# Optimization experiments

Measured on AMD Instinct MI355X. Metric: run time of the kernel, lower is better.

The kernel has to match this reference:

```python
import jax, jax.numpy as jnp
import numpy as np

A_BITS = 8   # activation fake-quant bits
W_BITS = 4   # weight fake-quant bits

H, I = 4096, 11008          # hidden / intermediate (LLaMA-7B)
UP_L, UP_R = 64, 64         # get_decompose_dim(4096)
DN_L, DN_R = 86, 128        # get_decompose_dim(11008)


def _round_ste(x):
    # straight-through rounding (fake quant)
    return x + jax.lax.stop_gradient(jnp.round(x) - x)


def fake_quant(x, bits, axis):
    """Symmetric fake quantization with dynamic max scaling along `axis`."""
    qmax = 2.0 ** (bits - 1) - 1.0
    s = jnp.max(jnp.abs(x), axis=axis, keepdims=True) / qmax
    s = jnp.maximum(s, 1e-8)
    q = jnp.clip(_round_ste(x / s), -qmax - 1.0, qmax)
    return q * s


def kron_trans(x, L, R, diag):
    """FlatQuant Kronecker-decomposed transform: x_ts = (x * diag) @ kron(L, R).
    Implemented as reshape to (l, r), L^T X R, reshape back."""
    shape = x.shape
    l, r = L.shape[0], R.shape[0]
    xr = (x * diag).reshape(*shape[:-1], l, r)
    y = jnp.einsum('...ij,ip,jq->...pq', xr, L, R)  # L^T X R
    return y.reshape(shape)


def inv_trans_weight(W, L, R, diag):
    """Transform weight rows by T^{-T} (T = diag * kron(L,R)) so that
    (x T) @ W_t^T == x @ W^T. W: [out, in]."""
    o, n = W.shape
    l, r = L.shape[0], R.shape[0]
    Wr = (W / diag).reshape(o, l, r)
    Li = jnp.linalg.inv(L)
    Ri = jnp.linalg.inv(R)
    Wt = jnp.einsum('pi,oij,qj->opq', Li, Wr, Ri)  # L^{-1} W' R^{-T}
    return Wt.reshape(o, n)


def setup_inputs() -> dict:
    key = jax.random.key(0)
    ks = jax.random.split(key, 10)
    B, S = 2, 2048

    def ortho(k, n):
        return jnp.linalg.qr(jax.random.normal(k, (n, n), jnp.float32))[0]

    x = jax.random.normal(ks[0], (B, S, H), jnp.float32)
    w_up = jax.random.normal(ks[1], (I, H), jnp.float32) * 0.02
    w_gate = jax.random.normal(ks[2], (I, H), jnp.float32) * 0.02
    w_down = jax.random.normal(ks[3], (H, I), jnp.float32) * 0.02
    up_L = ortho(ks[4], UP_L)
    up_R = ortho(ks[5], UP_R)
    up_diag = jax.random.uniform(ks[6], (H,), jnp.float32, 0.5, 1.5)
    dn_L = ortho(ks[7], DN_L)
    dn_R = ortho(ks[8], DN_R)
    dn_diag = jax.random.uniform(ks[9], (I,), jnp.float32, 0.5, 1.5)
    return {"x": x, "w_up": w_up, "w_gate": w_gate, "w_down": w_down,
            "up_L": up_L, "up_R": up_R, "up_diag": up_diag,
            "dn_L": dn_L, "dn_R": dn_R, "dn_diag": dn_diag}


def reference(x, w_up, w_gate, w_down, up_L, up_R, up_diag, dn_L, dn_R, dn_diag):
    # up/gate branch: transform -> quantize activation -> quantized linears
    x_ts = kron_trans(x, up_L, up_R, up_diag)                 # [B,S,H]
    xq = fake_quant(x_ts, A_BITS, -1)                         # per-token A8
    wu = fake_quant(inv_trans_weight(w_up, up_L, up_R, up_diag), W_BITS, 1)
    wg = fake_quant(inv_trans_weight(w_gate, up_L, up_R, up_diag), W_BITS, 1)
    up = jnp.einsum('bsh,ih->bsi', xq, wu)                    # [B,S,I]
    gate = jnp.einsum('bsh,ih->bsi', xq, wg)
    h = jax.nn.silu(gate) * up                                # SwiGLU
    # down branch
    h_ts = kron_trans(h, dn_L, dn_R, dn_diag)                 # [B,S,I]
    hq = fake_quant(h_ts, A_BITS, -1)
    wd = fake_quant(inv_trans_weight(w_down, dn_L, dn_R, dn_diag), W_BITS, 1)
    return jnp.einsum('bsi,hi->bsh', hq, wd)                  # [B,S,H]
```

## Files before the change

### kernel.cpp

```cpp
#include <hip/hip_runtime.h>
#include <hip/hip_bf16.h>
#include <math.h>

typedef __bf16 bf16x8 __attribute__((ext_vector_type(8)));
typedef float f32x4 __attribute__((ext_vector_type(4)));

#define TOK 4096
#define HDIM 4096
#define IDIM 11008

__global__ __launch_bounds__(256) void t64_kernel(
    const float* __restrict__ src, const float* __restrict__ Lm,
    const float* __restrict__ Rm, const float* __restrict__ diag,
    __hip_bfloat16* __restrict__ outq, float* __restrict__ scales,
    int mulDiag, float qmax, float qlo, float qhi)
{
    __shared__ float X[64 * 68];
    __shared__ float M1[64 * 68];
    __shared__ float LR[64 * 68];
    const int tid = threadIdx.x;
    const int row = blockIdx.x;
    const float* srow = src + (size_t)row * 4096;

    for (int idx = tid; idx < 4096; idx += 256) {
        float d = diag[idx];
        float v = srow[idx];
        v = mulDiag ? v * d : v / d;
        X[(idx >> 6) * 68 + (idx & 63)] = v;
        LR[(idx >> 6) * 68 + (idx & 63)] = Lm[idx];
    }
    __syncthreads();

    const int p0 = (tid >> 4) << 2;
    const int j0 = (tid & 15) << 2;

    float acc[4][4] = {};
    for (int i = 0; i < 64; ++i) {
        float a[4];
#pragma unroll
        for (int ii = 0; ii < 4; ++ii) a[ii] = LR[i * 68 + p0 + ii];
        float4 b = *(const float4*)&X[i * 68 + j0];
        float bv[4] = {b.x, b.y, b.z, b.w};
#pragma unroll
        for (int ii = 0; ii < 4; ++ii)
#pragma unroll
            for (int jj = 0; jj < 4; ++jj) acc[ii][jj] += a[ii] * bv[jj];
    }
#pragma unroll
    for (int ii = 0; ii < 4; ++ii)
        *(float4*)&M1[(p0 + ii) * 68 + j0] =
            make_float4(acc[ii][0], acc[ii][1], acc[ii][2], acc[ii][3]);
    __syncthreads();

    for (int idx = tid; idx < 4096; idx += 256)
        LR[(idx >> 6) * 68 + (idx & 63)] = Rm[idx];
    __syncthreads();

    float acc2[4][4] = {};
    for (int j = 0; j < 64; ++j) {
        float a[4];
#pragma unroll
        for (int ii = 0; ii < 4; ++ii) a[ii] = M1[(p0 + ii) * 68 + j];
        float4 b = *(const float4*)&LR[j * 68 + j0];
        float bv[4] = {b.x, b.y, b.z, b.w};
#pragma unroll
        for (int ii = 0; ii < 4; ++ii)
#pragma unroll
            for (int jj = 0; jj < 4; ++jj) acc2[ii][jj] += a[ii] * bv[jj];
    }

    float lm = 0.f;
#pragma unroll
    for (int ii = 0; ii < 4; ++ii)
#pragma unroll
        for (int jj = 0; jj < 4; ++jj) lm = fmaxf(lm, fabsf(acc2[ii][jj]));
    X[tid] = lm;
    __syncthreads();
    for (int s = 128; s > 0; s >>= 1) {
        if (tid < s) X[tid] = fmaxf(X[tid], X[tid + s]);
        __syncthreads();
    }
    const float sc = fmaxf(X[0] / qmax, 1e-8f);

#pragma unroll
    for (int ii = 0; ii < 4; ++ii)
#pragma unroll
        for (int jj = 0; jj < 4; ++jj) {
            float q = rintf(acc2[ii][jj] / sc);
            q = fminf(fmaxf(q, qlo), qhi);
            outq[(size_t)row * 4096 + (p0 + ii) * 64 + (j0 + jj)] =
                __float2bfloat16(q);
        }
    if (tid == 0) scales[row] = sc;
}

__global__ __launch_bounds__(512) void tdn_kernel(
    const void* __restrict__ src, int srcIsBf16,
    const float* __restrict__ Lm, const float* __restrict__ Rm,
    const float* __restrict__ diag,
    __hip_bfloat16* __restrict__ outq, float* __restrict__ scales,
    int mulDiag, float qmax, float qlo, float qhi)
{
    extern __shared__ float dsm[];
    float* X  = dsm;
    float* M1 = dsm + 11352;
    float* LR = dsm + 22704;
    __shared__ float red[512];

    const int tid = threadIdx.x;
    const int row = blockIdx.x;

    for (int idx = tid; idx < IDIM; idx += 512) {
        float v = srcIsBf16
            ? __bfloat162float(((const __hip_bfloat16*)src)[(size_t)row * IDIM + idx])
            : ((const float*)src)[(size_t)row * IDIM + idx];
        float d = diag[idx];
        v = mulDiag ? v * d : v / d;
        X[(idx >> 7) * 132 + (idx & 127)] = v;
    }
    for (int idx = tid; idx < 86 * 86; idx += 512) {
        int r = idx / 86, c = idx - r * 86;
        LR[r * 88 + c] = Lm[idx];
    }
    __syncthreads();

    for (int tt = tid; tt < 1376; tt += 512) {
        const int pp = (tt >> 5) * 2;
        const int jj0 = (tt & 31) * 4;
        float acc[2][4] = {};
        for (int i = 0; i < 86; ++i) {
            float a0 = LR[i * 88 + pp];
            float a1 = LR[i * 88 + pp + 1];
            float4 b = *(const float4*)&X[i * 132 + jj0];
            acc[0][0] += a0 * b.x; acc[0][1] += a0 * b.y;
            acc[0][2] += a0 * b.z; acc[0][3] += a0 * b.w;
            acc[1][0] += a1 * b.x; acc[1][1] += a1 * b.y;
            acc[1][2] += a1 * b.z; acc[1][3] += a1 * b.w;
        }
        *(float4*)&M1[pp * 132 + jj0] =
            make_float4(acc[0][0], acc[0][1], acc[0][2], acc[0][3]);
        *(float4*)&M1[(pp + 1) * 132 + jj0] =
            make_float4(acc[1][0], acc[1][1], acc[1][2], acc[1][3]);
    }
    __syncthreads();

    for (int idx = tid; idx < 128 * 128; idx += 512) {
        int r = idx >> 7, c = idx & 127;
        LR[r * 132 + c] = Rm[idx];
    }
    __syncthreads();

    float lm = 0.f;
    for (int tt = tid; tt < 1376; tt += 512) {
        const int pp = (tt >> 5) * 2;
        const int q0 = (tt & 31) * 4;
        float acc[2][4] = {};
        for (int j = 0; j < 128; ++j) {
            float a0 = M1[pp * 132 + j];
            float a1 = M1[(pp + 1) * 132 + j];
            float4 b = *(const float4*)&LR[j * 132 + q0];
            acc[0][0] += a0 * b.x; acc[0][1] += a0 * b.y;
            acc[0][2] += a0 * b.z; acc[0][3] += a0 * b.w;
            acc[1][0] += a1 * b.x; acc[1][1] += a1 * b.y;
            acc[1][2] += a1 * b.z; acc[1][3] += a1 * b.w;
        }
        *(float4*)&X[pp * 132 + q0] =
            make_float4(acc[0][0], acc[0][1], acc[0][2], acc[0][3]);
        *(float4*)&X[(pp + 1) * 132 + q0] =
            make_float4(acc[1][0], acc[1][1], acc[1][2], acc[1][3]);
#pragma unroll
        for (int ii = 0; ii < 2; ++ii)
#pragma unroll
            for (int qq = 0; qq < 4; ++qq) lm = fmaxf(lm, fabsf(acc[ii][qq]));
    }
    red[tid] = lm;
    __syncthreads();
    for (int s = 256; s > 0; s >>= 1) {
        if (tid < s) red[tid] = fmaxf(red[tid], red[tid + s]);
        __syncthreads();
    }
    const float sc = fmaxf(red[0] / qmax, 1e-8f);

    for (int idx = tid; idx < IDIM; idx += 512) {
        float v = X[(idx >> 7) * 132 + (idx & 127)];
        float q = rintf(v / sc);
        q = fminf(fmaxf(q, qlo), qhi);
        outq[(size_t)row * IDIM + idx] = __float2bfloat16(q);
    }
    if (tid == 0) scales[row] = sc;
}

__device__ __forceinline__ void gload16(const __hip_bfloat16* gsrc,
                                        __hip_bfloat16* ldst)
{
    __builtin_amdgcn_global_load_lds(
        (const __attribute__((address_space(1))) unsigned int*)gsrc,
        (__attribute__((address_space(3))) unsigned int*)ldst, 16, 0, 0);
}

template <bool DUAL>
__global__ __launch_bounds__(256, 2) void gemm_kernel(
    const __hip_bfloat16* __restrict__ A,
    const __hip_bfloat16* __restrict__ B0,
    const __hip_bfloat16* __restrict__ B1,
    const float* __restrict__ sA,
    const float* __restrict__ sB0,
    const float* __restrict__ sB1,
    int K,
    __hip_bfloat16* __restrict__ outH,
    float* __restrict__ outF,
    int outLd)
{
    constexpr int NT = DUAL ? 3 : 2;
    constexpr int TSZ = 128 * 64;
    __shared__ __align__(16) __hip_bfloat16 smem[NT * TSZ];

    const int tid = threadIdx.x;
    const int lane = tid & 63;
    const int lane15 = lane & 15;
    const int quad = lane >> 4;
    const int wave = tid >> 6;
    const int wr = wave >> 1;
    const int wc = wave & 1;
    const int n0 = blockIdx.x * 128;
    const int m0 = blockIdx.y * 128;

    const int srow = lane >> 3;
    const int scol = (lane & 7) * 8;

    f32x4 acc0[4][4] = {};
    f32x4 acc1[4][4] = {};

    const __hip_bfloat16* gA  = A + (size_t)m0 * K;
    const __hip_bfloat16* gB0 = B0 + (size_t)n0 * K;
    const __hip_bfloat16* gB1 = DUAL ? (B1 + (size_t)n0 * K) : nullptr;

    for (int kk = 0; kk < K; kk += 64) {
#pragma unroll
        for (int c = 0; c < 4; ++c) {
            const int r0 = wave * 32 + c * 8;
            gload16(gA + (size_t)(r0 + srow) * K + kk + scol,
                    smem + r0 * 64);
            gload16(gB0 + (size_t)(r0 + srow) * K + kk + scol,
                    smem + TSZ + r0 * 64);
            if constexpr (DUAL)
                gload16(gB1 + (size_t)(r0 + srow) * K + kk + scol,
                        smem + 2 * TSZ + r0 * 64);
        }
        __syncthreads();

#pragma unroll
        for (int ks = 0; ks < 2; ++ks) {
            const int kb = ks * 32 + quad * 8;
            bf16x8 af[4];
#pragma unroll
            for (int m = 0; m < 4; ++m)
                af[m] = *(const bf16x8*)(smem +
                         (wr * 64 + m * 16 + lane15) * 64 + kb);
#pragma unroll
            for (int c = 0; c < 4; ++c) {
                bf16x8 b0 = *(const bf16x8*)(smem + TSZ +
                             (wc * 64 + c * 16 + lane15) * 64 + kb);
#pragma unroll
                for (int m = 0; m < 4; ++m)
                    acc0[m][c] = __builtin_amdgcn_mfma_f32_16x16x32_bf16(
                        af[m], b0, acc0[m][c], 0, 0, 0);
                if constexpr (DUAL) {
                    bf16x8 b1 = *(const bf16x8*)(smem + 2 * TSZ +
                                 (wc * 64 + c * 16 + lane15) * 64 + kb);
#pragma unroll
                    for (int m = 0; m < 4; ++m)
                        acc1[m][c] = __builtin_amdgcn_mfma_f32_16x16x32_bf16(
                            af[m], b1, acc1[m][c], 0, 0, 0);
                }
            }
        }
        __syncthreads();
    }

#pragma unroll
    for (int m = 0; m < 4; ++m) {
        const int r0 = m0 + wr * 64 + m * 16 + quad * 4;
        float sa[4];
#pragma unroll
        for (int r = 0; r < 4; ++r) sa[r] = sA[r0 + r];
#pragma unroll
        for (int c = 0; c < 4; ++c) {
            const int col = n0 + wc * 64 + c * 16 + lane15;
            if constexpr (DUAL) {
                const float s0 = sB0[col], s1 = sB1[col];
#pragma unroll
                for (int r = 0; r < 4; ++r) {
                    float up = acc0[m][c][r] * (sa[r] * s0);
                    float gt = acc1[m][c][r] * (sa[r] * s1);
                    float hv = up * (gt / (1.f + __expf(-gt)));
                    outH[(size_t)(r0 + r) * outLd + col] = __float2bfloat16(hv);
                }
            } else {
                const float s0 = sB0[col];
#pragma unroll
                for (int r = 0; r < 4; ++r)
                    outF[(size_t)(r0 + r) * outLd + col] =
                        acc0[m][c][r] * (sa[r] * s0);
            }
        }
    }
}

extern "C" void kernel_launch(void* const* d_in, const int* in_sizes, int n_in,
                              void* d_out, int out_size, void* d_ws, size_t ws_size,
                              hipStream_t stream)
{
    const float* x       = (const float*)d_in[0];
    const float* w_up    = (const float*)d_in[1];
    const float* w_gate  = (const float*)d_in[2];
    const float* w_down  = (const float*)d_in[3];
    const float* up_L    = (const float*)d_in[4];
    const float* up_R    = (const float*)d_in[5];
    const float* up_diag = (const float*)d_in[6];
    const float* dn_L    = (const float*)d_in[7];
    const float* dn_R    = (const float*)d_in[8];
    const float* dn_diag = (const float*)d_in[9];
    float* out = (float*)d_out;

    char* w = (char*)d_ws;
    size_t off = 0;
    auto take = [&](size_t b) { char* p = w + off; off += (b + 255) & ~(size_t)255; return p; };
    __hip_bfloat16* wuq = (__hip_bfloat16*)take((size_t)IDIM * HDIM * 2);
    __hip_bfloat16* wgq = (__hip_bfloat16*)take((size_t)IDIM * HDIM * 2);
    __hip_bfloat16* wdq = (__hip_bfloat16*)take((size_t)HDIM * IDIM * 2);
    __hip_bfloat16* xq  = (__hip_bfloat16*)take((size_t)TOK * HDIM * 2);
    __hip_bfloat16* hq  = (__hip_bfloat16*)take((size_t)TOK * IDIM * 2);
    float* sx = (float*)take(TOK * 4);
    float* su = (float*)take(IDIM * 4);
    float* sg = (float*)take(IDIM * 4);
    float* sh = (float*)take(TOK * 4);
    float* sd = (float*)take(HDIM * 4);
    (void)in_sizes; (void)n_in; (void)out_size; (void)ws_size;

    const size_t tdn_lds = (size_t)(11352 + 11352 + 16896) * sizeof(float);
    hipFuncSetAttribute(reinterpret_cast<const void*>(&tdn_kernel),
                        hipFuncAttributeMaxDynamicSharedMemorySize, (int)tdn_lds);

    t64_kernel<<<TOK,  256, 0, stream>>>(x,      up_L, up_R, up_diag, xq,  sx, 1, 127.f, -128.f, 127.f);
    t64_kernel<<<IDIM, 256, 0, stream>>>(w_up,   up_L, up_R, up_diag, wuq, su, 0, 7.f,   -8.f,   7.f);
    t64_kernel<<<IDIM, 256, 0, stream>>>(w_gate, up_L, up_R, up_diag, wgq, sg, 0, 7.f,   -8.f,   7.f);
    tdn_kernel<<<HDIM, 512, tdn_lds, stream>>>(w_down, 0, dn_L, dn_R, dn_diag, wdq, sd, 0, 7.f, -8.f, 7.f);

    gemm_kernel<true><<<dim3(IDIM / 128, TOK / 128), 256, 0, stream>>>(
        xq, wuq, wgq, sx, su, sg, HDIM, hq, nullptr, IDIM);

    tdn_kernel<<<TOK, 512, tdn_lds, stream>>>(hq, 1, dn_L, dn_R, dn_diag, hq, sh, 1, 127.f, -128.f, 127.f);

    gemm_kernel<false><<<dim3(HDIM / 128, TOK / 128), 256, 0, stream>>>(
        hq, wdq, nullptr, sh, sd, nullptr, IDIM, nullptr, out, HDIM);
}
```

Before: 3.586 ms.

## Vectorize and retile Kronecker transform kernels with transposed intermediate layout

Rewrites the per-row Kronecker transform kernels to use float4 global loads and packed bf16 stores. The first-stage result is stored transposed so the second matmul reads float4 operands instead of scalar strided ones. The 11008-wide kernel moves to 256 threads, each computing a 4x8 register tile, which raises arithmetic per LDS load and changes the LDS layout. Register pressure and occupancy trade-offs may shift, and the GEMMs, which likely dominate total time, are unchanged.

```diff
diff --git a/kernel.cpp b/kernel.cpp
--- a/kernel.cpp
+++ b/kernel.cpp
@@ -8,6 +8,14 @@
 #define TOK 4096
 #define HDIM 4096
 #define IDIM 11008
+
+__device__ __forceinline__ unsigned int bf16bits(float f)
+{
+    __hip_bfloat16 h = __float2bfloat16(f);
+    union { __hip_bfloat16 h; unsigned short u; } cv;
+    cv.h = h;
+    return (unsigned int)cv.u;
+}
 
 __global__ __launch_bounds__(256) void t64_kernel(
     const float* __restrict__ src, const float* __restrict__ Lm,
@@ -22,12 +30,16 @@
     const int row = blockIdx.x;
     const float* srow = src + (size_t)row * 4096;
 
-    for (int idx = tid; idx < 4096; idx += 256) {
-        float d = diag[idx];
-        float v = srow[idx];
-        v = mulDiag ? v * d : v / d;
-        X[(idx >> 6) * 68 + (idx & 63)] = v;
-        LR[(idx >> 6) * 68 + (idx & 63)] = Lm[idx];
+    for (int i4 = tid; i4 < 1024; i4 += 256) {
+        const int idx = i4 * 4;
+        float4 d = *(const float4*)(diag + idx);
+        float4 v = *(const float4*)(srow + idx);
+        float4 l = *(const float4*)(Lm + idx);
+        if (mulDiag) { v.x *= d.x; v.y *= d.y; v.z *= d.z; v.w *= d.w; }
+        else         { v.x /= d.x; v.y /= d.y; v.z /= d.z; v.w /= d.w; }
+        const int r = idx >> 6, c = idx & 63;
+        *(float4*)&X[r * 68 + c] = v;
+        *(float4*)&LR[r * 68 + c] = l;
     }
     __syncthreads();
 
@@ -35,38 +47,36 @@
     const int j0 = (tid & 15) << 2;
 
     float acc[4][4] = {};
+#pragma unroll 2
     for (int i = 0; i < 64; ++i) {
-        float a[4];
-#pragma unroll
-        for (int ii = 0; ii < 4; ++ii) a[ii] = LR[i * 68 + p0 + ii];
+        float4 a = *(const float4*)&LR[i * 68 + p0];
         float4 b = *(const float4*)&X[i * 68 + j0];
-        float bv[4] = {b.x, b.y, b.z, b.w};
-#pragma unroll
-        for (int ii = 0; ii < 4; ++ii)
-#pragma unroll
-            for (int jj = 0; jj < 4; ++jj) acc[ii][jj] += a[ii] * bv[jj];
-    }
-#pragma unroll
-    for (int ii = 0; ii < 4; ++ii)
-        *(float4*)&M1[(p0 + ii) * 68 + j0] =
-            make_float4(acc[ii][0], acc[ii][1], acc[ii][2], acc[ii][3]);
-    __syncthreads();
-
-    for (int idx = tid; idx < 4096; idx += 256)
-        LR[(idx >> 6) * 68 + (idx & 63)] = Rm[idx];
+        acc[0][0] += a.x * b.x; acc[0][1] += a.x * b.y; acc[0][2] += a.x * b.z; acc[0][3] += a.x * b.w;
+        acc[1][0] += a.y * b.x; acc[1][1] += a.y * b.y; acc[1][2] += a.y * b.z; acc[1][3] += a.y * b.w;
+        acc[2][0] += a.z * b.x; acc[2][1] += a.z * b.y; acc[2][2] += a.z * b.z; acc[2][3] += a.z * b.w;
+        acc[3][0] += a.w * b.x; acc[3][1] += a.w * b.y; acc[3][2] += a.w * b.z; acc[3][3] += a.w * b.w;
+    }
+#pragma unroll
+    for (int jj = 0; jj < 4; ++jj)
+        *(float4*)&M1[(j0 + jj) * 68 + p0] =
+            make_float4(acc[0][jj], acc[1][jj], acc[2][jj], acc[3][jj]);
+    __syncthreads();
+
+    for (int i4 = tid; i4 < 1024; i4 += 256) {
+        const int idx = i4 * 4;
+        *(float4*)&LR[(idx >> 6) * 68 + (idx & 63)] = *(const float4*)(Rm + idx);
+    }
     __syncthreads();
 
     float acc2[4][4] = {};
+#pragma unroll 2
     for (int j = 0; j < 64; ++j) {
-        float a[4];
-#pragma unroll
-        for (int ii = 0; ii < 4; ++ii) a[ii] = M1[(p0 + ii) * 68 + j];
+        float4 a = *(const float4*)&M1[j * 68 + p0];
         float4 b = *(const float4*)&LR[j * 68 + j0];
-        float bv[4] = {b.x, b.y, b.z, b.w};
-#pragma unroll
-        for (int ii = 0; ii < 4; ++ii)
-#pragma unroll
-            for (int jj = 0; jj < 4; ++jj) acc2[ii][jj] += a[ii] * bv[jj];
+        acc2[0][0] += a.x * b.x; acc2[0][1] += a.x * b.y; acc2[0][2] += a.x * b.z; acc2[0][3] += a.x * b.w;
+        acc2[1][0] += a.y * b.x; acc2[1][1] += a.y * b.y; acc2[1][2] += a.y * b.z; acc2[1][3] += a.y * b.w;
+        acc2[2][0] += a.z * b.x; acc2[2][1] += a.z * b.y; acc2[2][2] += a.z * b.z; acc2[2][3] += a.z * b.w;
+        acc2[3][0] += a.w * b.x; acc2[3][1] += a.w * b.y; acc2[3][2] += a.w * b.z; acc2[3][3] += a.w * b.w;
     }
 
     float lm = 0.f;
@@ -83,18 +93,23 @@
     const float sc = fmaxf(X[0] / qmax, 1e-8f);
 
 #pragma unroll
-    for (int ii = 0; ii < 4; ++ii)
-#pragma unroll
-        for (int jj = 0; jj < 4; ++jj) {
-            float q = rintf(acc2[ii][jj] / sc);
-            q = fminf(fmaxf(q, qlo), qhi);
-            outq[(size_t)row * 4096 + (p0 + ii) * 64 + (j0 + jj)] =
-                __float2bfloat16(q);
-        }
+    for (int ii = 0; ii < 4; ++ii) {
+        unsigned int lo, hi;
+        {
+            float q0 = fminf(fmaxf(rintf(acc2[ii][0] / sc), qlo), qhi);
+            float q1 = fminf(fmaxf(rintf(acc2[ii][1] / sc), qlo), qhi);
+            float q2 = fminf(fmaxf(rintf(acc2[ii][2] / sc), qlo), qhi);
+            float q3 = fminf(fmaxf(rintf(acc2[ii][3] / sc), qlo), qhi);
+            lo = bf16bits(q0) | (bf16bits(q1) << 16);
+            hi = bf16bits(q2) | (bf16bits(q3) << 16);
+        }
+        *(uint2*)(outq + (size_t)row * 4096 + (p0 + ii) * 64 + j0) =
+            make_uint2(lo, hi);
+    }
     if (tid == 0) scales[row] = sc;
 }
 
-__global__ __launch_bounds__(512) void tdn_kernel(
+__global__ __launch_bounds__(256) void tdn_kernel(
     const void* __restrict__ src, int srcIsBf16,
     const float* __restrict__ Lm, const float* __restrict__ Rm,
     const float* __restrict__ diag,
@@ -103,89 +118,115 @@
 {
     extern __shared__ float dsm[];
     float* X  = dsm;
-    float* M1 = dsm + 11352;
-    float* LR = dsm + 22704;
-    __shared__ float red[512];
+    float* M1 = dsm + 11616;
+    float* LR = dsm + 22880;
+    __shared__ float red[256];
 
     const int tid = threadIdx.x;
     const int row = blockIdx.x;
 
-    for (int idx = tid; idx < IDIM; idx += 512) {
-        float v = srcIsBf16
-            ? __bfloat162float(((const __hip_bfloat16*)src)[(size_t)row * IDIM + idx])
-            : ((const float*)src)[(size_t)row * IDIM + idx];
-        float d = diag[idx];
-        v = mulDiag ? v * d : v / d;
-        X[(idx >> 7) * 132 + (idx & 127)] = v;
-    }
-    for (int idx = tid; idx < 86 * 86; idx += 512) {
-        int r = idx / 86, c = idx - r * 86;
-        LR[r * 88 + c] = Lm[idx];
-    }
-    __syncthreads();
-
-    for (int tt = tid; tt < 1376; tt += 512) {
-        const int pp = (tt >> 5) * 2;
-        const int jj0 = (tt & 31) * 4;
-        float acc[2][4] = {};
+    for (int i4 = tid; i4 < IDIM / 4; i4 += 256) {
+        const int idx = i4 * 4;
+        float4 v;
+        if (srcIsBf16) {
+            uint2 raw = *(const uint2*)((const unsigned short*)src +
+                                        (size_t)row * IDIM + idx);
+            v.x = __uint_as_float(raw.x << 16);
+            v.y = __uint_as_float(raw.x & 0xffff0000u);
+            v.z = __uint_as_float(raw.y << 16);
+            v.w = __uint_as_float(raw.y & 0xffff0000u);
+        } else {
+            v = *(const float4*)((const float*)src + (size_t)row * IDIM + idx);
+        }
+        float4 d = *(const float4*)(diag + idx);
+        if (mulDiag) { v.x *= d.x; v.y *= d.y; v.z *= d.z; v.w *= d.w; }
+        else         { v.x /= d.x; v.y /= d.y; v.z /= d.z; v.w /= d.w; }
+        *(float4*)&X[(idx >> 7) * 132 + (idx & 127)] = v;
+    }
+    for (int idx = tid; idx < 86 * 88; idx += 256) {
+        const int r = idx / 88, c = idx - r * 88;
+        LR[idx] = (c < 86) ? Lm[r * 86 + c] : 0.f;
+    }
+    __syncthreads();
+
+    for (int tt = tid; tt < 352; tt += 256) {
+        const int pp = (tt >> 4) << 2;
+        const int jb = (tt & 15) << 3;
+        float acc[4][8] = {};
+#pragma unroll 2
         for (int i = 0; i < 86; ++i) {
-            float a0 = LR[i * 88 + pp];
-            float a1 = LR[i * 88 + pp + 1];
-            float4 b = *(const float4*)&X[i * 132 + jj0];
-            acc[0][0] += a0 * b.x; acc[0][1] += a0 * b.y;
-            acc[0][2] += a0 * b.z; acc[0][3] += a0 * b.w;
-            acc[1][0] += a1 * b.x; acc[1][1] += a1 * b.y;
-            acc[1][2] += a1 * b.z; acc[1][3] += a1 * b.w;
-        }
-        *(float4*)&M1[pp * 132 + jj0] =
-            make_float4(acc[0][0], acc[0][1], acc[0][2], acc[0][3]);
-        *(float4*)&M1[(pp + 1) * 132 + jj0] =
-            make_float4(acc[1][0], acc[1][1], acc[1][2], acc[1][3]);
-    }
-    __syncthreads();
-
-    for (int idx = tid; idx < 128 * 128; idx += 512) {
-        int r = idx >> 7, c = idx & 127;
-        LR[r * 132 + c] = Rm[idx];
+            float4 a  = *(const float4*)&LR[i * 88 + pp];
+            float4 b0 = *(const float4*)&X[i * 132 + jb];
+            float4 b1 = *(const float4*)&X[i * 132 + jb + 4];
+            acc[0][0] += a.x * b0.x; acc[0][1] += a.x * b0.y; acc[0][2] += a.x * b0.z; acc[0][3] += a.x * b0.w;
+            acc[0][4] += a.x * b1.x; acc[0][5] += a.x * b1.y; acc[0][6] += a.x * b1.z; acc[0][7] += a.x * b1.w;
+            acc[1][0] += a.y * b0.x; acc[1][1] += a.y * b0.y; acc[1][2] += a.y * b0.z; acc[1][3] += a.y * b0.w;
+            acc[1][4] += a.y * b1.x; acc[1][5] += a.y * b1.y; acc[1][6] += a.y * b1.z; acc[1][7] += a.y * b1.w;
+            acc[2][0] += a.z * b0.x; acc[2][1] += a.z * b0.y; acc[2][2] += a.z * b0.z; acc[2][3] += a.z * b0.w;
+            acc[2][4] += a.z * b1.x; acc[2][5] += a.z * b1.y; acc[2][6] += a.z * b1.z; acc[2][7] += a.z * b1.w;
+            acc[3][0] += a.w * b0.x; acc[3][1] += a.w * b0.y; acc[3][2] += a.w * b0.z; acc[3][3] += a.w * b0.w;
+            acc[3][4] += a.w * b1.x; acc[3][5] += a.w * b1.y; acc[3][6] += a.w * b1.z; acc[3][7] += a.w * b1.w;
+        }
+#pragma unroll
+        for (int jj = 0; jj < 8; ++jj)
+            *(float4*)&M1[(jb + jj) * 88 + pp] =
+                make_float4(acc[0][jj], acc[1][jj], acc[2][jj], acc[3][jj]);
+    }
+    __syncthreads();
+
+    for (int i4 = tid; i4 < 4096; i4 += 256) {
+        const int idx = i4 * 4;
+        *(float4*)&LR[(idx >> 7) * 132 + (idx & 127)] = *(const float4*)(Rm + idx);
     }
     __syncthreads();
 
     float lm = 0.f;
-    for (int tt = tid; tt < 1376; tt += 512) {
-        const int pp = (tt >> 5) * 2;
-        const int q0 = (tt & 31) * 4;
-        float acc[2][4] = {};
+    for (int tt = tid; tt < 352; tt += 256) {
+        const int pp = (tt >> 4) << 2;
+        const int qb = (tt & 15) << 3;
+        float acc[4][8] = {};
+#pragma unroll 2
         for (int j = 0; j < 128; ++j) {
-            float a0 = M1[pp * 132 + j];
-            float a1 = M1[(pp + 1) * 132 + j];
-            float4 b = *(const float4*)&LR[j * 132 + q0];
-            acc[0][0] += a0 * b.x; acc[0][1] += a0 * b.y;
-            acc[0][2] += a0 * b.z; acc[0][3] += a0 * b.w;
-            acc[1][0] += a1 * b.x; acc[1][1] += a1 * b.y;
-            acc[1][2] += a1 * b.z; acc[1][3] += a1 * b.w;
-        }
-        *(float4*)&X[pp * 132 + q0] =
-            make_float4(acc[0][0], acc[0][1], acc[0][2], acc[0][3]);
-        *(float4*)&X[(pp + 1) * 132 + q0] =
-            make_float4(acc[1][0], acc[1][1], acc[1][2], acc[1][3]);
-#pragma unroll
-        for (int ii = 0; ii < 2; ++ii)
-#pragma unroll
-            for (int qq = 0; qq < 4; ++qq) lm = fmaxf(lm, fabsf(acc[ii][qq]));
+            float4 a  = *(const float4*)&M1[j * 88 + pp];
+            float4 b0 = *(const float4*)&LR[j * 132 + qb];
+            float4 b1 = *(const float4*)&LR[j * 132 + qb + 4];
+            acc[0][0] += a.x * b0.x; acc[0][1] += a.x * b0.y; acc[0][2] += a.x * b0.z; acc[0][3] += a.x * b0.w;
+            acc[0][4] += a.x * b1.x; acc[0][5] += a.x * b1.y; acc[0][6] += a.x * b1.z; acc[0][7] += a.x * b1.w;
+            acc[1][0] += a.y * b0.x; acc[1][1] += a.y * b0.y; acc[1][2] += a.y * b0.z; acc[1][3] += a.y * b0.w;
+            acc[1][4] += a.y * b1.x; acc[1][5] += a.y * b1.y; acc[1][6] += a.y * b1.z; acc[1][7] += a.y * b1.w;
+            acc[2][0] += a.z * b0.x; acc[2][1] += a.z * b0.y; acc[2][2] += a.z * b0.z; acc[2][3] += a.z * b0.w;
+            acc[2][4] += a.z * b1.x; acc[2][5] += a.z * b1.y; acc[2][6] += a.z * b1.z; acc[2][7] += a.z * b1.w;
+            acc[3][0] += a.w * b0.x; acc[3][1] += a.w * b0.y; acc[3][2] += a.w * b0.z; acc[3][3] += a.w * b0.w;
+            acc[3][4] += a.w * b1.x; acc[3][5] += a.w * b1.y; acc[3][6] += a.w * b1.z; acc[3][7] += a.w * b1.w;
+        }
+#pragma unroll
+        for (int ii = 0; ii < 4; ++ii) {
+            *(float4*)&X[(pp + ii) * 132 + qb] =
+                make_float4(acc[ii][0], acc[ii][1], acc[ii][2], acc[ii][3]);
+            *(float4*)&X[(pp + ii) * 132 + qb + 4] =
+                make_float4(acc[ii][4], acc[ii][5], acc[ii][6], acc[ii][7]);
+#pragma unroll
+            for (int qq = 0; qq < 8; ++qq) lm = fmaxf(lm, fabsf(acc[ii][qq]));
+        }
     }
     red[tid] = lm;
     __syncthreads();
-    for (int s = 256; s > 0; s >>= 1) {
+    for (int s = 128; s > 0; s >>= 1) {
         if (tid < s) red[tid] = fmaxf(red[tid], red[tid + s]);
         __syncthreads();
     }
     const float sc = fmaxf(red[0] / qmax, 1e-8f);
 
-    for (int idx = tid; idx < IDIM; idx += 512) {
-        float v = X[(idx >> 7) * 132 + (idx & 127)];
-        float q = rintf(v / sc);
-        q = fminf(fmaxf(q, qlo), qhi);
-        outq[(size_t)row * IDIM + idx] = __float2bfloat16(q);
+    for (int i4 = tid; i4 < IDIM / 4; i4 += 256) {
+        const int idx = i4 * 4;
+        float4 v = *(const float4*)&X[(idx >> 7) * 132 + (idx & 127)];
+        float q0 = fminf(fmaxf(rintf(v.x / sc), qlo), qhi);
+        float q1 = fminf(fmaxf(rintf(v.y / sc), qlo), qhi);
+        float q2 = fminf(fmaxf(rintf(v.z / sc), qlo), qhi);
+        float q3 = fminf(fmaxf(rintf(v.w / sc), qlo), qhi);
+        unsigned int lo = bf16bits(q0) | (bf16bits(q1) << 16);
+        unsigned int hi = bf16bits(q2) | (bf16bits(q3) << 16);
+        *(uint2*)(outq + (size_t)row * IDIM + idx) = make_uint2(lo, hi);
     }
     if (tid == 0) scales[row] = sc;
 }
@@ -338,19 +379,19 @@
     float* sd = (float*)take(HDIM * 4);
     (void)in_sizes; (void)n_in; (void)out_size; (void)ws_size;
 
-    const size_t tdn_lds = (size_t)(11352 + 11352 + 16896) * sizeof(float);
+    const size_t tdn_lds = (size_t)(11616 + 11264 + 16896) * sizeof(float);
     hipFuncSetAttribute(reinterpret_cast<const void*>(&tdn_kernel),
                         hipFuncAttributeMaxDynamicSharedMemorySize, (int)tdn_lds);
 
     t64_kernel<<<TOK,  256, 0, stream>>>(x,      up_L, up_R, up_diag, xq,  sx, 1, 127.f, -128.f, 127.f);
     t64_kernel<<<IDIM, 256, 0, stream>>>(w_up,   up_L, up_R, up_diag, wuq, su, 0, 7.f,   -8.f,   7.f);
     t64_kernel<<<IDIM, 256, 0, stream>>>(w_gate, up_L, up_R, up_diag, wgq, sg, 0, 7.f,   -8.f,   7.f);
-    tdn_kernel<<<HDIM, 512, tdn_lds, stream>>>(w_down, 0, dn_L, dn_R, dn_diag, wdq, sd, 0, 7.f, -8.f, 7.f);
+    tdn_kernel<<<HDIM, 256, tdn_lds, stream>>>(w_down, 0, dn_L, dn_R, dn_diag, wdq, sd, 0, 7.f, -8.f, 7.f);
 
     gemm_kernel<true><<<dim3(IDIM / 128, TOK / 128), 256, 0, stream>>>(
         xq, wuq, wgq, sx, su, sg, HDIM, hq, nullptr, IDIM);
 
-    tdn_kernel<<<TOK, 512, tdn_lds, stream>>>(hq, 1, dn_L, dn_R, dn_diag, hq, sh, 1, 127.f, -128.f, 127.f);
+    tdn_kernel<<<TOK, 256, tdn_lds, stream>>>(hq, 1, dn_L, dn_R, dn_diag, hq, sh, 1, 127.f, -128.f, 127.f);
 
     gemm_kernel<false><<<dim3(HDIM / 128, TOK / 128), 256, 0, stream>>>(
         hq, wdq, nullptr, sh, sd, nullptr, IDIM, nullptr, out, HDIM);
```

After: 3.545 ms. About the same (-1.1%).
